# Kernel optimization log

Measured on AMD Instinct MI355X. Metric: run time of the kernel, lower is better.

## Reference

```python
import jax, jax.numpy as jnp
from jax import lax
import numpy as np

B, S, D, H, L, DFF = 64, 512, 512, 8, 6, 2048
CLIP_C = 10.0
EPS = 1e-5


def setup_inputs() -> dict:
    key = jax.random.key(0)
    ks = jax.random.split(key, 16)
    sc = 0.02
    inp = {
        "x": jax.random.normal(ks[0], (B, S, D), jnp.float32),
        "mask": jnp.zeros((B, S, S), jnp.float32),
        # stacked per-layer params [L, ...]; Linear stored as (out, in) like torch
        "qkv_w": jax.random.normal(ks[1], (L, 3 * D, D), jnp.float32) * sc,
        "qkv_b": jnp.zeros((L, 3 * D), jnp.float32),
        "ln1_g": jnp.ones((L, D), jnp.float32),
        "ln1_b": jnp.zeros((L, D), jnp.float32),
        "kv_w": jax.random.normal(ks[2], (L, 2 * D, D), jnp.float32) * sc,
        "kv_b": jnp.zeros((L, 2 * D), jnp.float32),
        "ln2_g": jnp.ones((L, D), jnp.float32),
        "ln2_b": jnp.zeros((L, D), jnp.float32),
        "w1": jax.random.normal(ks[3], (L, DFF, D), jnp.float32) * sc,
        "b1": jnp.zeros((L, DFF), jnp.float32),
        "w2": jax.random.normal(ks[4], (L, D, DFF), jnp.float32) * sc,
        "b2": jnp.zeros((L, D), jnp.float32),
        "ln3_g": jnp.ones((L, D), jnp.float32),
        "ln3_b": jnp.zeros((L, D), jnp.float32),
    }
    return inp


def _ln(v, g, b):
    m = v.mean(-1, keepdims=True)
    var = ((v - m) ** 2).mean(-1, keepdims=True)
    return (v - m) * lax.rsqrt(var + EPS) * g + b


def _mha(q, k, v, mask, clip_c):
    # faithful to custom_multi_head_attn: bmm -> /sqrt(hd) -> [c*tanh] -> +mask -> softmax -> bmm
    b, sq, d = q.shape
    sk = k.shape[1]
    hd = d // H
    qh = q.reshape(b, sq, H, hd)
    kh = k.reshape(b, sk, H, hd)
    vh = v.reshape(b, sk, H, hd)
    s = jnp.einsum('bqhd,bkhd->bhqk', qh, kh) * (1.0 / float(hd) ** 0.5)
    if clip_c is not None:
        s = clip_c * jnp.tanh(s)
    if mask is not None:
        s = s + mask[:, None]  # repeat over heads
    a = jax.nn.softmax(s, axis=-1)
    return jnp.einsum('bhqk,bkhd->bqhd', a, vh).reshape(b, sq, d)


def reference(x, mask, qkv_w, qkv_b, ln1_g, ln1_b, kv_w, kv_b, ln2_g, ln2_b,
              w1, b1, w2, b2, ln3_g, ln3_b):
    def step(h, p):
        (qw, qb, g1, be1, kw, kb, g2, be2, fw1, fb1, fw2, fb2, g3, be3) = p
        # self-attention block (no FFN, no mask, no clip; note: NO out-projection,
        # matching the original which never applies out_proj_weight)
        qkv = h @ qw.T + qb
        q, k, v = jnp.split(qkv, 3, axis=-1)
        x1 = _ln(h + _mha(q, k, v, None, None), g1, be1)
        # cross-attention block: query = sa output (no q_proj), kv from original h
        kv_ = h @ kw.T + kb
        k2, v2 = jnp.split(kv_, 2, axis=-1)
        y = _ln(x1 + _mha(x1, k2, v2, mask, CLIP_C), g2, be2)
        # FFN + residual + norm (post-norm)
        ff = jax.nn.relu(y @ fw1.T + fb1) @ fw2.T + fb2
        return _ln(y + ff, g3, be3), None

    params = (qkv_w, qkv_b, ln1_g, ln1_b, kv_w, kv_b, ln2_g, ln2_b,
              w1, b1, w2, b2, ln3_g, ln3_b)
    out, _ = lax.scan(step, x, params)
    return out
```

## Files before the change

### kernel.cpp

```cpp
#include <hip/hip_runtime.h>


typedef __bf16 bf16_t;
typedef __bf16 bf16x8 __attribute__((ext_vector_type(8)));
typedef __bf16 bf16x4 __attribute__((ext_vector_type(4)));
typedef float  f32x4  __attribute__((ext_vector_type(4)));

#define NB   64
#define NS   512
#define ND   512
#define NH   8
#define NHD  64
#define NL   6
#define NDFF 2048
#define NM   (NB * NS)

__device__ __forceinline__ void gld_lds16(const void* gsrc, void* lds) {
  __builtin_amdgcn_global_load_lds((__attribute__((address_space(1))) void*)gsrc,
                                   (__attribute__((address_space(3))) void*)lds,
                                   16, 0, 0);
}

template<int N> __device__ __forceinline__ void vm_wait() {
  if constexpr (N == 0)      asm volatile("s_waitcnt vmcnt(0)" ::: "memory");
  else if constexpr (N == 8) asm volatile("s_waitcnt vmcnt(8)" ::: "memory");
}
__device__ __forceinline__ void lgkm0() {
  asm volatile("s_waitcnt lgkmcnt(0)" ::: "memory");
}

__global__ __launch_bounds__(256) void cvt_f32_bf16(const float* __restrict__ in,
                                                    bf16_t* __restrict__ out,
                                                    long n) {
  long i = ((long)blockIdx.x * 256 + threadIdx.x) * 8;
  const long stride = (long)gridDim.x * 256 * 8;
  for (; i < n; i += stride) {
    f32x4 a = *(const f32x4*)(in + i);
    f32x4 b = *(const f32x4*)(in + i + 4);
    bf16x8 o;
#pragma unroll
    for (int j = 0; j < 4; ++j) { o[j] = (bf16_t)a[j]; o[j + 4] = (bf16_t)b[j]; }
    *(bf16x8*)(out + i) = o;
  }
}

template<bool RELU, bool BIAS_ROW>
__global__ __launch_bounds__(256) void gemm97(const bf16_t* __restrict__ Ap,
                                              const bf16_t* __restrict__ Wp,
                                              const float* __restrict__ bias,
                                              bf16_t* __restrict__ Cout,
                                              int Nn, int Kk) {
  __shared__ __attribute__((aligned(16))) bf16_t As[2][128 * 64];
  __shared__ __attribute__((aligned(16))) bf16_t Bs[2][128 * 64];
  const int tid = threadIdx.x;
  const int l   = tid & 63;
  const int w   = tid >> 6;
  const int wr  = (w >> 1) * 64;
  const int wc  = (w & 1) * 64;
  const int l15 = l & 15, lg = l >> 4;

  const int nn   = Nn >> 7;
  const int nwg  = gridDim.x;
  const int flat = blockIdx.x;
  const int wgid = (nwg & 7) ? flat : (flat & 7) * (nwg >> 3) + (flat >> 3);
  const int m0 = (wgid / nn) * 128;
  const int n0 = (wgid % nn) * 128;

  const int prow = w * 32 + (l >> 3);

  auto stage = [&](int kt, int bf_) {
    const int kc = kt * 64;
#pragma unroll
    for (int i = 0; i < 4; ++i) {
      const int rA = prow + i * 8;
      const int g  = (l & 7) ^ (rA & 7);
      gld_lds16(Ap + (size_t)(m0 + rA) * Kk + kc + g * 8, &As[bf_][(w * 4 + i) * 512]);
    }
#pragma unroll
    for (int i = 0; i < 4; ++i) {
      const int rB = prow + i * 8;
      const int g  = (l & 7) ^ (rB & 7);
      gld_lds16(Wp + (size_t)(n0 + rB) * Kk + kc + g * 8, &Bs[bf_][(w * 4 + i) * 512]);
    }
  };
  auto ldA = [&](int bf_, int mi, int kk) -> bf16x8 {
    const int row = wr + mi * 16 + l15;
    return *(const bf16x8*)&As[bf_][row * 64 + (((kk * 4 + lg) ^ (row & 7)) * 8)];
  };
  auto ldB = [&](int bf_, int ni, int kk) -> bf16x8 {
    const int row = wc + ni * 16 + l15;
    return *(const bf16x8*)&Bs[bf_][row * 64 + (((kk * 4 + lg) ^ (row & 7)) * 8)];
  };

  f32x4 acc[4][4];
#pragma unroll
  for (int i = 0; i < 4; ++i)
#pragma unroll
    for (int j = 0; j < 4; ++j) acc[i][j] = (f32x4){0.f, 0.f, 0.f, 0.f};

  const int KT = Kk >> 6;
  stage(0, 0);

  int buf = 0;
  for (int kt = 0; kt < KT; ++kt) {
    if (kt + 1 < KT) { stage(kt + 1, buf ^ 1); vm_wait<8>(); }
    else             vm_wait<0>();
    __builtin_amdgcn_s_barrier();
#pragma unroll
    for (int kk = 0; kk < 2; ++kk) {
      bf16x8 af[4], bw[4];
#pragma unroll
      for (int i = 0; i < 4; ++i) { af[i] = ldA(buf, i, kk); bw[i] = ldB(buf, i, kk); }
      __builtin_amdgcn_s_setprio(1);
#pragma unroll
      for (int mi = 0; mi < 4; ++mi)
#pragma unroll
        for (int ni = 0; ni < 4; ++ni)
          acc[mi][ni] = __builtin_amdgcn_mfma_f32_16x16x32_bf16(af[mi], bw[ni], acc[mi][ni], 0, 0, 0);
      __builtin_amdgcn_s_setprio(0);
    }
    lgkm0();
    __builtin_amdgcn_s_barrier();
    buf ^= 1;
  }

#pragma unroll
  for (int mi = 0; mi < 4; ++mi)
#pragma unroll
    for (int ni = 0; ni < 4; ++ni) {
      const int col = n0 + wc + ni * 16 + l15;
      const float bc = BIAS_ROW ? 0.f : bias[col];
#pragma unroll
      for (int r = 0; r < 4; ++r) {
        const int rowi = m0 + wr + mi * 16 + lg * 4 + r;
        float v = acc[mi][ni][r] + (BIAS_ROW ? bias[rowi] : bc);
        if (RELU) v = fmaxf(v, 0.f);
        Cout[(size_t)rowi * Nn + col] = (bf16_t)v;
      }
    }
}

template<int CROSS, bool M16>
__global__ __launch_bounds__(256, 2) void attn6(const bf16_t* __restrict__ Q,
                                                const bf16_t* __restrict__ K,
                                                const bf16_t* __restrict__ Vt,
                                                const void* __restrict__ maskp,
                                                bf16_t* __restrict__ O,
                                                int qstride, int kstride, int vstride) {
  __shared__ __attribute__((aligned(16))) bf16_t k_s[2][64 * 64];
  __shared__ __attribute__((aligned(16))) bf16_t v_s[2][64 * 64];
  __shared__ __attribute__((aligned(16))) bf16_t p_s[64 * 64];

  const int tid = threadIdx.x;
  const int l   = tid & 63;
  const int w   = tid >> 6;
  const int bid = blockIdx.x;
  const int h   = bid & 7;
  const int qt  = (bid >> 3) & 7;
  const int b   = bid >> 6;
  const int h64 = h * NHD;
  const int l15 = l & 15, lg = l >> 4;

  const float FM = CROSS ? 10.f : 16.f;
  const int qglob = qt * 64 + w * 16 + l15;

  auto stageK = [&](int kt, int buf) {
#pragma unroll
    for (int i = 0; i < 2; ++i) {
      const int r  = i * 32 + (tid >> 3);
      const int c8 = (tid & 7) ^ (r & 7);
      gld_lds16(K + (size_t)(b * NS + kt * 64 + r) * kstride + h64 + c8 * 8,
                &k_s[buf][(i * 32 + w * 8) * 64]);
    }
  };
  auto stageV = [&](int kt, int buf) {
#pragma unroll
    for (int i = 0; i < 2; ++i) {
      const int d = i * 32 + (tid >> 3);
      const int g = (tid & 7) ^ (d & 7);
      gld_lds16(Vt + (size_t)(h64 + d) * vstride + b * NS + kt * 64 + g * 8,
                &v_s[buf][(i * 32 + w * 8) * 64]);
    }
  };

  stageK(0, 0); stageV(0, 0);

  bf16x8 qf[2];
#pragma unroll
  for (int c = 0; c < 2; ++c)
    qf[c] = *(const bf16x8*)(Q + (size_t)(b * NS + qglob) * qstride + h64 + c * 32 + lg * 8);

  bf16x4 mk16[2][4];
  f32x4  mkf[2][4];
  if (CROSS) {
#pragma unroll
    for (int nt = 0; nt < 4; ++nt) {
      if (M16) mk16[0][nt] = *(const bf16x4*)((const bf16_t*)maskp
                              + (size_t)(b * NS + qglob) * NS + nt * 16 + lg * 4);
      else     mkf[0][nt]  = *(const f32x4*)((const float*)maskp
                              + (size_t)(b * NS + qglob) * NS + nt * 16 + lg * 4);
    }
  }

  float l_run = 0.f;
  const f32x4 zz = {0.f, 0.f, 0.f, 0.f};
  f32x4 oacc[4] = {zz, zz, zz, zz};

#pragma unroll
  for (int kt = 0; kt < 8; ++kt) {
    const int buf = kt & 1;
    __syncthreads();
    if (kt < 7) {
      stageK(kt + 1, buf ^ 1);
      stageV(kt + 1, buf ^ 1);
      if (CROSS) {
#pragma unroll
        for (int nt = 0; nt < 4; ++nt) {
          if (M16) mk16[buf ^ 1][nt] = *(const bf16x4*)((const bf16_t*)maskp
                     + (size_t)(b * NS + qglob) * NS + (kt + 1) * 64 + nt * 16 + lg * 4);
          else     mkf[buf ^ 1][nt]  = *(const f32x4*)((const float*)maskp
                     + (size_t)(b * NS + qglob) * NS + (kt + 1) * 64 + nt * 16 + lg * 4);
        }
      }
    }

    f32x4 s[4];
    __builtin_amdgcn_s_setprio(1);
#pragma unroll
    for (int nt = 0; nt < 4; ++nt) {
      const int row = nt * 16 + l15;
      bf16x8 ka0 = *(const bf16x8*)((const char*)k_s[buf] + row * 128 + ((lg ^ (row & 7)) * 16));
      bf16x8 ka1 = *(const bf16x8*)((const char*)k_s[buf] + row * 128 + (((4 + lg) ^ (row & 7)) * 16));
      f32x4 z = zz;
      z = __builtin_amdgcn_mfma_f32_16x16x32_bf16(ka0, qf[0], z, 0, 0, 0);
      z = __builtin_amdgcn_mfma_f32_16x16x32_bf16(ka1, qf[1], z, 0, 0, 0);
      s[nt] = z;
    }
    __builtin_amdgcn_s_setprio(0);

    float ts = 0.f;
    const int prow = w * 16 + l15;
#pragma unroll
    for (int nt = 0; nt < 4; ++nt) {
      f32x4 v = s[nt] * 0.125f;
      bf16x4 pk;
#pragma unroll
      for (int r = 0; r < 4; ++r) {
        float sv = v[r];
        if (CROSS) {
          const float e2 = __expf(2.f * sv);
          const float mkv = M16 ? (float)mk16[buf][nt][r] : mkf[buf][nt][r];
          sv = 10.f - 20.f * __builtin_amdgcn_rcpf(e2 + 1.f) + mkv;
        }
        const float e = __expf(sv - FM);
        ts += e;
        pk[r] = (bf16_t)e;
      }
      const int gran = (nt * 2 + (lg >> 1)) ^ (prow & 7);
      *(bf16x4*)((char*)p_s + prow * 128 + gran * 16 + (lg & 1) * 8) = pk;
    }
    l_run += ts;

    __builtin_amdgcn_s_setprio(1);
#pragma unroll
    for (int ks = 0; ks < 2; ++ks) {
      const int ag = (ks * 4 + lg) ^ (prow & 7);
      bf16x8 pa = *(const bf16x8*)((const char*)p_s + prow * 128 + ag * 16);
#pragma unroll
      for (int dt = 0; dt < 4; ++dt) {
        const int vrow = dt * 16 + l15;
        const int vg   = (ks * 4 + lg) ^ (vrow & 7);
        bf16x8 vb = *(const bf16x8*)((const char*)v_s[buf] + vrow * 128 + vg * 16);
        oacc[dt] = __builtin_amdgcn_mfma_f32_16x16x32_bf16(pa, vb, oacc[dt], 0, 0, 0);
      }
    }
    __builtin_amdgcn_s_setprio(0);
  }

  l_run += __shfl_xor(l_run, 16, 64);
  l_run += __shfl_xor(l_run, 32, 64);
  const float inv = 1.f / l_run;
  float invq[4];
#pragma unroll
  for (int r = 0; r < 4; ++r) invq[r] = __shfl(inv, lg * 4 + r, 64);
#pragma unroll
  for (int dt = 0; dt < 4; ++dt)
#pragma unroll
    for (int r = 0; r < 4; ++r) {
      const size_t row = (size_t)(b * NS + qt * 64 + w * 16 + lg * 4 + r);
      O[row * ND + h64 + dt * 16 + l15] = (bf16_t)(oacc[dt][r] * invq[r]);
    }
}

template<bool A16, bool W32>
__global__ __launch_bounds__(256) void add_ln2(const void* __restrict__ Xav,
                                               const bf16_t* __restrict__ Xb,
                                               const float* __restrict__ gw,
                                               const float* __restrict__ bw,
                                               float* __restrict__ o32,
                                               bf16_t* __restrict__ o16) {
  const int l = threadIdx.x & 63;
  const size_t row  = (size_t)blockIdx.x * 4 + (threadIdx.x >> 6);
  const size_t base = row * ND + l * 8;
  f32x4 a0, a1;
  if (A16) {
    bf16x8 t = *(const bf16x8*)((const bf16_t*)Xav + base);
#pragma unroll
    for (int i = 0; i < 4; ++i) { a0[i] = (float)t[i]; a1[i] = (float)t[i + 4]; }
  } else {
    a0 = *(const f32x4*)((const float*)Xav + base);
    a1 = *(const f32x4*)((const float*)Xav + base + 4);
  }
  bf16x8 tb = *(const bf16x8*)(Xb + base);
  f32x4 b0, b1;
#pragma unroll
  for (int i = 0; i < 4; ++i) { b0[i] = (float)tb[i]; b1[i] = (float)tb[i + 4]; }
  f32x4 v0 = a0 + b0, v1 = a1 + b1;
  float s = v0[0] + v0[1] + v0[2] + v0[3] + v1[0] + v1[1] + v1[2] + v1[3];
#pragma unroll
  for (int off = 1; off < 64; off <<= 1) s += __shfl_xor(s, off, 64);
  const float mean = s * (1.f / ND);
  f32x4 d0 = v0 - mean, d1 = v1 - mean;
  float q = d0[0]*d0[0] + d0[1]*d0[1] + d0[2]*d0[2] + d0[3]*d0[3]
          + d1[0]*d1[0] + d1[1]*d1[1] + d1[2]*d1[2] + d1[3]*d1[3];
#pragma unroll
  for (int off = 1; off < 64; off <<= 1) q += __shfl_xor(q, off, 64);
  const float rstd = rsqrtf(q * (1.f / ND) + 1e-5f);
  const f32x4 g0 = *(const f32x4*)(gw + l * 8), g1 = *(const f32x4*)(gw + l * 8 + 4);
  const f32x4 h0 = *(const f32x4*)(bw + l * 8), h1 = *(const f32x4*)(bw + l * 8 + 4);
  f32x4 r0 = d0 * rstd * g0 + h0;
  f32x4 r1 = d1 * rstd * g1 + h1;
  if (W32) {
    *(f32x4*)(o32 + base)     = r0;
    *(f32x4*)(o32 + base + 4) = r1;
  } else {
    bf16x8 o;
#pragma unroll
    for (int i = 0; i < 4; ++i) { o[i] = (bf16_t)r0[i]; o[i + 4] = (bf16_t)r1[i]; }
    *(bf16x8*)(o16 + base) = o;
  }
}

extern "C" void kernel_launch(void* const* d_in, const int* in_sizes, int n_in,
                              void* d_out, int out_size, void* d_ws, size_t ws_size,
                              hipStream_t stream) {
  (void)in_sizes; (void)n_in; (void)out_size;
  const float* x     = (const float*)d_in[0];
  const float* maskp = (const float*)d_in[1];
  const float* qkvw  = (const float*)d_in[2];
  const float* qkvb  = (const float*)d_in[3];
  const float* ln1g  = (const float*)d_in[4];
  const float* ln1b  = (const float*)d_in[5];
  const float* kvw   = (const float*)d_in[6];
  const float* kvb   = (const float*)d_in[7];
  const float* ln2g  = (const float*)d_in[8];
  const float* ln2b  = (const float*)d_in[9];
  const float* w1p   = (const float*)d_in[10];
  const float* b1p   = (const float*)d_in[11];
  const float* w2p   = (const float*)d_in[12];
  const float* b2p   = (const float*)d_in[13];
  const float* ln3g  = (const float*)d_in[14];
  const float* ln3b  = (const float*)d_in[15];
  float* out = (float*)d_out;

  const size_t WALL = 40894464, WLYR = 6815744, H16B = 33554432, M16B = 33554432;
  struct Tier { int R; bool allw; };
  const Tier tiers[6] = {{32768, true}, {16384, true}, {8192, true},
                         {4096, true}, {2048, false}, {1024, false}};
  int R = 0; bool allw = false; size_t base_need = 0;
  for (int t = 0; t < 6; ++t) {
    size_t need = (tiers[t].allw ? WALL : WLYR) + H16B +
                  (size_t)tiers[t].R * 7168 + 16384;
    if (ws_size >= need) { R = tiers[t].R; allw = tiers[t].allw; base_need = need; break; }
  }
  if (R == 0) return;
  const bool m16 = (ws_size >= base_need + M16B + 256);
  const int nchunks = NM / R;
  const int CB = R / NS;
  const int MT = R / 128;

  char* p = (char*)d_ws;
  auto alloc = [&](size_t bytes) { char* r = p; p += (bytes + 255) & ~(size_t)255; return r; };
  bf16_t* WQ = (bf16_t*)alloc((allw ? NL : 1) * (size_t)1536 * ND * 2);
  bf16_t* WK = (bf16_t*)alloc((allw ? NL : 1) * (size_t)1024 * ND * 2);
  bf16_t* W1 = (bf16_t*)alloc((allw ? NL : 1) * (size_t)NDFF * ND * 2);
  bf16_t* W2 = (bf16_t*)alloc((allw ? NL : 1) * (size_t)ND * NDFF * 2);
  bf16_t* h16  = (bf16_t*)alloc((size_t)NM * ND * 2);
  bf16_t* big  = (bf16_t*)alloc((size_t)R * NDFF * 2);
  bf16_t* t16  = (bf16_t*)alloc((size_t)R * ND * 2);
  bf16_t* x116 = (bf16_t*)alloc((size_t)R * ND * 2);
  bf16_t* y16  = (bf16_t*)alloc((size_t)R * ND * 2);
  bf16_t* mask16 = m16 ? (bf16_t*)alloc(M16B) : nullptr;

  auto cvt = [&](const float* src, bf16_t* dst, long n) {
    int blocks = (int)((n / 8 + 255) / 256); if (blocks > 8192) blocks = 8192;
    hipLaunchKernelGGL(cvt_f32_bf16, dim3(blocks), dim3(256), 0, stream, src, dst, n);
  };

  cvt(x, h16, (long)NM * ND);
  if (m16) cvt(maskp, mask16, (long)NM * NS);
  if (allw) {
    cvt(qkvw, WQ, (long)NL * 1536 * ND);
    cvt(kvw,  WK, (long)NL * 1024 * ND);
    cvt(w1p,  W1, (long)NL * NDFF * ND);
    cvt(w2p,  W2, (long)NL * ND * NDFF);
  }

  for (int l = 0; l < NL; ++l) {
    const bf16_t *wq_l, *wk_l, *w1_l, *w2_l;
    if (allw) {
      wq_l = WQ + (size_t)l * 1536 * ND;
      wk_l = WK + (size_t)l * 1024 * ND;
      w1_l = W1 + (size_t)l * NDFF * ND;
      w2_l = W2 + (size_t)l * ND * NDFF;
    } else {
      cvt(qkvw + (size_t)l * 1536 * ND, WQ, (long)1536 * ND);
      cvt(kvw  + (size_t)l * 1024 * ND, WK, (long)1024 * ND);
      cvt(w1p  + (size_t)l * NDFF * ND, W1, (long)NDFF * ND);
      cvt(w2p  + (size_t)l * ND * NDFF, W2, (long)ND * NDFF);
      wq_l = WQ; wk_l = WK; w1_l = W1; w2_l = W2;
    }

    for (int c = 0; c < nchunks; ++c) {
      const size_t r0 = (size_t)c * R;
      bf16_t*       h16c  = h16 + r0 * ND;
      bf16_t* vtS = big + (size_t)R * 1024;
      bf16_t* vtC = big + (size_t)R * 512;

      hipLaunchKernelGGL(HIP_KERNEL_NAME(gemm97<false, false>), dim3(MT * 8), dim3(256), 0, stream,
                         h16c, wq_l, qkvb + l * 1536, big, 1024, 512);
      hipLaunchKernelGGL(HIP_KERNEL_NAME(gemm97<false, true>), dim3(MT * 4), dim3(256), 0, stream,
                         wq_l + (size_t)1024 * 512, h16c, qkvb + l * 1536 + 1024, vtS, R, 512);
      hipLaunchKernelGGL(HIP_KERNEL_NAME(attn6<0, false>), dim3(CB * 64), dim3(256), 0, stream,
                         big, big + 512, vtS, (const void*)nullptr, t16, 1024, 1024, R);
      if (l == 0)
        hipLaunchKernelGGL(HIP_KERNEL_NAME(add_ln2<false, false>), dim3(R / 4), dim3(256), 0, stream,
                           (const void*)(x + r0 * ND), t16, ln1g, ln1b, (float*)nullptr, x116);
      else
        hipLaunchKernelGGL(HIP_KERNEL_NAME(add_ln2<true, false>), dim3(R / 4), dim3(256), 0, stream,
                           (const void*)h16c, t16, ln1g + l * ND, ln1b + l * ND, (float*)nullptr, x116);
      hipLaunchKernelGGL(HIP_KERNEL_NAME(gemm97<false, false>), dim3(MT * 4), dim3(256), 0, stream,
                         h16c, wk_l, kvb + l * 1024, big, 512, 512);
      hipLaunchKernelGGL(HIP_KERNEL_NAME(gemm97<false, true>), dim3(MT * 4), dim3(256), 0, stream,
                         wk_l + (size_t)512 * 512, h16c, kvb + l * 1024 + 512, vtC, R, 512);
      if (m16)
        hipLaunchKernelGGL(HIP_KERNEL_NAME(attn6<1, true>), dim3(CB * 64), dim3(256), 0, stream,
                           x116, big, vtC, (const void*)(mask16 + r0 * NS), t16, 512, 512, R);
      else
        hipLaunchKernelGGL(HIP_KERNEL_NAME(attn6<1, false>), dim3(CB * 64), dim3(256), 0, stream,
                           x116, big, vtC, (const void*)(maskp + r0 * NS), t16, 512, 512, R);
      hipLaunchKernelGGL(HIP_KERNEL_NAME(add_ln2<true, false>), dim3(R / 4), dim3(256), 0, stream,
                         (const void*)x116, t16, ln2g + l * ND, ln2b + l * ND, (float*)nullptr, y16);
      hipLaunchKernelGGL(HIP_KERNEL_NAME(gemm97<true, false>), dim3(MT * 16), dim3(256), 0, stream,
                         y16, w1_l, b1p + l * NDFF, big, 2048, 512);
      hipLaunchKernelGGL(HIP_KERNEL_NAME(gemm97<false, false>), dim3(MT * 4), dim3(256), 0, stream,
                         big, w2_l, b2p + l * ND, t16, 512, 2048);
      if (l < NL - 1)
        hipLaunchKernelGGL(HIP_KERNEL_NAME(add_ln2<true, false>), dim3(R / 4), dim3(256), 0, stream,
                           (const void*)y16, t16, ln3g + l * ND, ln3b + l * ND, (float*)nullptr, h16c);
      else
        hipLaunchKernelGGL(HIP_KERNEL_NAME(add_ln2<true, true>), dim3(R / 4), dim3(256), 0, stream,
                           (const void*)y16, t16, ln3g + l * ND, ln3b + l * ND, out + r0 * ND, (bf16_t*)nullptr);
    }
  }
}
```

Measured before the change: 3.632 ms.

## Fuse self-attn QK and cross-attn K projections into one GEMM

Repacks the weights so the Q, K (self-attention) and K2 (cross-attention) projections form one 1536-wide weight matrix with a concatenated bias, all computed in a single GEMM over h. The two V transposed projections now run back to back before attention, with the cross-attention V stored in the y16 buffer, and the attention kernels read with a stride of 1536. This removes one GEMM launch and one extra read of the h chunk per layer and chunk, and makes the fused GEMM grid larger. In exchange it adds per-layer weight conversion launches, bias copies, more workspace, and a wider strided read in attention.

```diff
diff --git a/kernel.cpp b/kernel.cpp
--- a/kernel.cpp
+++ b/kernel.cpp
@@ -370,7 +370,7 @@
   int R = 0; bool allw = false; size_t base_need = 0;
   for (int t = 0; t < 6; ++t) {
     size_t need = (tiers[t].allw ? WALL : WLYR) + H16B +
-                  (size_t)tiers[t].R * 7168 + 16384;
+                  (size_t)tiers[t].R * 7168 + 131072;
     if (ws_size >= need) { R = tiers[t].R; allw = tiers[t].allw; base_need = need; break; }
   }
   if (R == 0) return;
@@ -381,10 +381,12 @@
 
   char* p = (char*)d_ws;
   auto alloc = [&](size_t bytes) { char* r = p; p += (bytes + 255) & ~(size_t)255; return r; };
-  bf16_t* WQ = (bf16_t*)alloc((allw ? NL : 1) * (size_t)1536 * ND * 2);
-  bf16_t* WK = (bf16_t*)alloc((allw ? NL : 1) * (size_t)1024 * ND * 2);
-  bf16_t* W1 = (bf16_t*)alloc((allw ? NL : 1) * (size_t)NDFF * ND * 2);
-  bf16_t* W2 = (bf16_t*)alloc((allw ? NL : 1) * (size_t)ND * NDFF * 2);
+  bf16_t* WQK = (bf16_t*)alloc((allw ? NL : 1) * (size_t)1536 * ND * 2);
+  bf16_t* WV  = (bf16_t*)alloc((allw ? NL : 1) * (size_t)512 * ND * 2);
+  bf16_t* WV2 = (bf16_t*)alloc((allw ? NL : 1) * (size_t)512 * ND * 2);
+  bf16_t* W1  = (bf16_t*)alloc((allw ? NL : 1) * (size_t)NDFF * ND * 2);
+  bf16_t* W2  = (bf16_t*)alloc((allw ? NL : 1) * (size_t)ND * NDFF * 2);
+  float*  bqk2 = (float*)alloc((size_t)NL * 1536 * 4);
   bf16_t* h16  = (bf16_t*)alloc((size_t)NM * ND * 2);
   bf16_t* big  = (bf16_t*)alloc((size_t)R * NDFF * 2);
   bf16_t* t16  = (bf16_t*)alloc((size_t)R * ND * 2);
@@ -396,59 +398,71 @@
     int blocks = (int)((n / 8 + 255) / 256); if (blocks > 8192) blocks = 8192;
     hipLaunchKernelGGL(cvt_f32_bf16, dim3(blocks), dim3(256), 0, stream, src, dst, n);
   };
+  auto cvt_layer = [&](int l, bf16_t* wqk, bf16_t* wv, bf16_t* wv2) {
+    cvt(qkvw + (size_t)l * 1536 * ND,                 wqk,                 (long)1024 * ND);
+    cvt(kvw  + (size_t)l * 1024 * ND,                 wqk + (size_t)1024 * ND, (long)512 * ND);
+    cvt(qkvw + (size_t)l * 1536 * ND + (size_t)1024 * ND, wv,              (long)512 * ND);
+    cvt(kvw  + (size_t)l * 1024 * ND + (size_t)512 * ND,  wv2,             (long)512 * ND);
+  };
+
+  for (int l = 0; l < NL; ++l) {
+    hipMemcpyAsync(bqk2 + (size_t)l * 1536,        qkvb + (size_t)l * 1536,
+                   1024 * sizeof(float), hipMemcpyDeviceToDevice, stream);
+    hipMemcpyAsync(bqk2 + (size_t)l * 1536 + 1024, kvb + (size_t)l * 1024,
+                   512 * sizeof(float), hipMemcpyDeviceToDevice, stream);
+  }
 
   cvt(x, h16, (long)NM * ND);
   if (m16) cvt(maskp, mask16, (long)NM * NS);
   if (allw) {
-    cvt(qkvw, WQ, (long)NL * 1536 * ND);
-    cvt(kvw,  WK, (long)NL * 1024 * ND);
-    cvt(w1p,  W1, (long)NL * NDFF * ND);
-    cvt(w2p,  W2, (long)NL * ND * NDFF);
+    for (int l = 0; l < NL; ++l)
+      cvt_layer(l, WQK + (size_t)l * 1536 * ND, WV + (size_t)l * 512 * ND,
+                WV2 + (size_t)l * 512 * ND);
+    cvt(w1p, W1, (long)NL * NDFF * ND);
+    cvt(w2p, W2, (long)NL * ND * NDFF);
   }
 
   for (int l = 0; l < NL; ++l) {
-    const bf16_t *wq_l, *wk_l, *w1_l, *w2_l;
+    const bf16_t *wqk_l, *wv_l, *wv2_l, *w1_l, *w2_l;
     if (allw) {
-      wq_l = WQ + (size_t)l * 1536 * ND;
-      wk_l = WK + (size_t)l * 1024 * ND;
-      w1_l = W1 + (size_t)l * NDFF * ND;
-      w2_l = W2 + (size_t)l * ND * NDFF;
+      wqk_l = WQK + (size_t)l * 1536 * ND;
+      wv_l  = WV  + (size_t)l * 512 * ND;
+      wv2_l = WV2 + (size_t)l * 512 * ND;
+      w1_l  = W1  + (size_t)l * NDFF * ND;
+      w2_l  = W2  + (size_t)l * ND * NDFF;
     } else {
-      cvt(qkvw + (size_t)l * 1536 * ND, WQ, (long)1536 * ND);
-      cvt(kvw  + (size_t)l * 1024 * ND, WK, (long)1024 * ND);
-      cvt(w1p  + (size_t)l * NDFF * ND, W1, (long)NDFF * ND);
-      cvt(w2p  + (size_t)l * ND * NDFF, W2, (long)ND * NDFF);
-      wq_l = WQ; wk_l = WK; w1_l = W1; w2_l = W2;
+      cvt_layer(l, WQK, WV, WV2);
+      cvt(w1p + (size_t)l * NDFF * ND, W1, (long)NDFF * ND);
+      cvt(w2p + (size_t)l * ND * NDFF, W2, (long)ND * NDFF);
+      wqk_l = WQK; wv_l = WV; wv2_l = WV2; w1_l = W1; w2_l = W2;
     }
 
     for (int c = 0; c < nchunks; ++c) {
       const size_t r0 = (size_t)c * R;
       bf16_t*       h16c  = h16 + r0 * ND;
-      bf16_t* vtS = big + (size_t)R * 1024;
-      bf16_t* vtC = big + (size_t)R * 512;
-
-      hipLaunchKernelGGL(HIP_KERNEL_NAME(gemm97<false, false>), dim3(MT * 8), dim3(256), 0, stream,
-                         h16c, wq_l, qkvb + l * 1536, big, 1024, 512);
+      bf16_t* vtS = big + (size_t)R * 1536;
+      bf16_t* vtC = y16;
+
+      hipLaunchKernelGGL(HIP_KERNEL_NAME(gemm97<false, false>), dim3(MT * 12), dim3(256), 0, stream,
+                         h16c, wqk_l, bqk2 + (size_t)l * 1536, big, 1536, 512);
       hipLaunchKernelGGL(HIP_KERNEL_NAME(gemm97<false, true>), dim3(MT * 4), dim3(256), 0, stream,
-                         wq_l + (size_t)1024 * 512, h16c, qkvb + l * 1536 + 1024, vtS, R, 512);
+                         wv_l, h16c, qkvb + l * 1536 + 1024, vtS, R, 512);
+      hipLaunchKernelGGL(HIP_KERNEL_NAME(gemm97<false, true>), dim3(MT * 4), dim3(256), 0, stream,
+                         wv2_l, h16c, kvb + l * 1024 + 512, vtC, R, 512);
       hipLaunchKernelGGL(HIP_KERNEL_NAME(attn6<0, false>), dim3(CB * 64), dim3(256), 0, stream,
-                         big, big + 512, vtS, (const void*)nullptr, t16, 1024, 1024, R);
+                         big, big + 512, vtS, (const void*)nullptr, t16, 1536, 1536, R);
       if (l == 0)
         hipLaunchKernelGGL(HIP_KERNEL_NAME(add_ln2<false, false>), dim3(R / 4), dim3(256), 0, stream,
                            (const void*)(x + r0 * ND), t16, ln1g, ln1b, (float*)nullptr, x116);
       else
         hipLaunchKernelGGL(HIP_KERNEL_NAME(add_ln2<true, false>), dim3(R / 4), dim3(256), 0, stream,
                            (const void*)h16c, t16, ln1g + l * ND, ln1b + l * ND, (float*)nullptr, x116);
-      hipLaunchKernelGGL(HIP_KERNEL_NAME(gemm97<false, false>), dim3(MT * 4), dim3(256), 0, stream,
-                         h16c, wk_l, kvb + l * 1024, big, 512, 512);
-      hipLaunchKernelGGL(HIP_KERNEL_NAME(gemm97<false, true>), dim3(MT * 4), dim3(256), 0, stream,
-                         wk_l + (size_t)512 * 512, h16c, kvb + l * 1024 + 512, vtC, R, 512);
       if (m16)
         hipLaunchKernelGGL(HIP_KERNEL_NAME(attn6<1, true>), dim3(CB * 64), dim3(256), 0, stream,
-                           x116, big, vtC, (const void*)(mask16 + r0 * NS), t16, 512, 512, R);
+                           x116, big + 1024, vtC, (const void*)(mask16 + r0 * NS), t16, 512, 1536, R);
       else
         hipLaunchKernelGGL(HIP_KERNEL_NAME(attn6<1, false>), dim3(CB * 64), dim3(256), 0, stream,
-                           x116, big, vtC, (const void*)(maskp + r0 * NS), t16, 512, 512, R);
+                           x116, big + 1024, vtC, (const void*)(maskp + r0 * NS), t16, 512, 1536, R);
       hipLaunchKernelGGL(HIP_KERNEL_NAME(add_ln2<true, false>), dim3(R / 4), dim3(256), 0, stream,
                          (const void*)x116, t16, ln2g + l * ND, ln2b + l * ND, (float*)nullptr, y16);
       hipLaunchKernelGGL(HIP_KERNEL_NAME(gemm97<true, false>), dim3(MT * 16), dim3(256), 0, stream,
```

After: 3.657 ms. About the same (+0.7%).
